# Kernel optimization log

Measured on AMD Instinct MI355X. Metric: run time of the kernel, lower is better.

## Reference

```python
import jax, jax.numpy as jnp
import numpy as np

EMBED = 512
HEADS = 8
HEAD_D = EMBED // HEADS
N = 16
QLEN = 512
KLEN = 512


def _relative_keys(Wr, q_len, k_len):
    # Transformer-XL style sinusoid table of size (q_len + k_len)
    max_dist = q_len + k_len
    inv_freqs = 10000.0 ** (-jnp.arange(0, EMBED, 2, dtype=jnp.float32) / EMBED)
    seq = jnp.arange(max_dist, dtype=jnp.float32)[:, None] * inv_freqs[None, :]
    pos_emb = jnp.concatenate([jnp.sin(seq), jnp.cos(seq)], axis=-1)  # [max_dist, E]
    rel = (pos_emb @ Wr.T).reshape(max_dist, HEADS, HEAD_D)           # [max_dist, H, D]
    # query_offset defaults to key_len
    q_pos = jnp.arange(q_len)[:, None] + k_len
    k_pos = jnp.arange(k_len)[None, :]
    rel_idx = jnp.clip(q_pos - k_pos, 0, max_dist - 1)                # [q, k]
    return rel[rel_idx]                                               # [q, k, H, D]


def setup_inputs() -> dict:
    key = jax.random.key(0)
    ks = jax.random.split(key, 12)
    s = 0.02
    return {
        "values": jax.random.normal(ks[0], (N, KLEN, EMBED), jnp.float32),
        "keys": jax.random.normal(ks[1], (N, KLEN, EMBED), jnp.float32),
        "query": jax.random.normal(ks[2], (N, QLEN, EMBED), jnp.float32),
        "mask": jnp.ones((N, QLEN, KLEN), jnp.int32),
        "Wv": jax.random.normal(ks[3], (HEAD_D, HEAD_D), jnp.float32) * s,
        "Wk": jax.random.normal(ks[4], (HEAD_D, HEAD_D), jnp.float32) * s,
        "Wq": jax.random.normal(ks[5], (HEAD_D, HEAD_D), jnp.float32) * s,
        "Wr": jax.random.normal(ks[6], (EMBED, EMBED), jnp.float32) * s,
        "u_bias": jax.random.normal(ks[7], (HEADS, HEAD_D), jnp.float32) * s,
        "v_bias": jax.random.normal(ks[8], (HEADS, HEAD_D), jnp.float32) * s,
        "Wo": jax.random.normal(ks[9], (EMBED, EMBED), jnp.float32) * s,
        "bo": jnp.zeros((EMBED,), jnp.float32),
    }


def reference(values, keys, query, mask, Wv, Wk, Wq, Wr, u_bias, v_bias, Wo, bo):
    # per-head projections (same D x D weight shared across heads, torch Linear: x @ W.T)
    v = values.reshape(N, KLEN, HEADS, HEAD_D) @ Wv.T
    k = keys.reshape(N, KLEN, HEADS, HEAD_D) @ Wk.T
    q = query.reshape(N, QLEN, HEADS, HEAD_D) @ Wq.T

    rel_keys = _relative_keys(Wr, QLEN, KLEN)  # [q, k, H, D]

    content = jnp.einsum("nqhd,nkhd->nhqk", q + u_bias, k)
    position = jnp.einsum("nqhd,qkhd->nhqk", q + v_bias, rel_keys)
    energy = content + position
    energy = jnp.where(mask[:, None, :, :] == 0, jnp.float32(-1e20), energy)

    attn = jax.nn.softmax(energy / (float(HEAD_D) ** 0.5), axis=3)  # [N,H,q,k]
    out = jnp.einsum("nhqk,nkhd->nqhd", attn, v).reshape(N, QLEN, EMBED)
    out = out @ Wo.T + bo
    return out, attn
```

## Files before the change

kernel.cpp:

```cpp
#include <hip/hip_runtime.h>
#include <math.h>

#define NB     16
#define HEADS  8
#define HD     64
#define EMBED  512
#define QL     512
#define KL     512

#define WS_QU   0
#define WS_QV   2097152
#define WS_KB   4194304
#define WS_VT   6291456
#define WS_PEB  8388608
#define WS_RELB 8912896
#define WS_OH   9175040

typedef __attribute__((ext_vector_type(8))) short bf16x8;
typedef __attribute__((ext_vector_type(4))) float f32x4;
typedef __attribute__((ext_vector_type(8))) unsigned short ushort8v;
typedef __attribute__((ext_vector_type(4))) unsigned short ushort4v;

#define MFMA16 __builtin_amdgcn_mfma_f32_16x16x32_bf16

static __device__ __forceinline__ unsigned short f2bf(float x) {
    unsigned u = __builtin_bit_cast(unsigned, x);
    u += 0x7fffu + ((u >> 16) & 1u);
    return (unsigned short)(u >> 16);
}

__global__ void pe_kernel(unsigned short* __restrict__ peb) {
    int j = blockIdx.x;
    int i = threadIdx.x;
    float invf = exp2f(-(float)i * (13.287712379549449f / 256.0f));
    float ang  = (float)j * invf;
    peb[j * 512 + i]       = f2bf(sinf(ang));
    peb[j * 512 + 256 + i] = f2bf(cosf(ang));
}

__global__ __launch_bounds__(256) void rel_kernel(const unsigned short* __restrict__ peb,
                                                  const float* __restrict__ Wr,
                                                  unsigned short* __restrict__ relb) {
    __shared__ __align__(16) unsigned short At[64][64];
    __shared__ __align__(16) unsigned short Bt[64][64];
    int bm = blockIdx.x >> 3, bn = blockIdx.x & 7;
    int tid = threadIdx.x;
    int w = tid >> 6, lane = tid & 63;
    int fr = lane & 15, fg = lane >> 4;
    f32x4 acc[4] = {};
    for (int kk = 0; kk < 512; kk += 64) {
        __syncthreads();
        for (int p = 0; p < 2; ++p) {
            int idx = tid + 256 * p;
            int row = idx >> 3, slot = idx & 7;
            *(bf16x8*)&At[row][((slot ^ (row & 7))) * 8] =
                *(const bf16x8*)&peb[(bm * 64 + row) * 512 + kk + slot * 8];
        }
        for (int p = 0; p < 4; ++p) {
            int idx = tid + 256 * p;
            int row = idx >> 4, c4 = idx & 15;
            float4 v = *(const float4*)&Wr[(bn * 64 + row) * 512 + kk + c4 * 4];
            ushort4v pk;
            pk[0] = f2bf(v.x); pk[1] = f2bf(v.y); pk[2] = f2bf(v.z); pk[3] = f2bf(v.w);
            int slot = c4 >> 1, rem = (c4 & 1) * 4;
            *(ushort4v*)&Bt[row][((slot ^ (row & 7))) * 8 + rem] = pk;
        }
        __syncthreads();
        bf16x8 af[2];
        int ar = w * 16 + fr;
#pragma unroll
        for (int s = 0; s < 2; ++s)
            af[s] = *(const bf16x8*)&At[ar][((fg + 4 * s) ^ (ar & 7)) * 8];
#pragma unroll
        for (int c = 0; c < 4; ++c) {
            int br = c * 16 + fr;
#pragma unroll
            for (int s = 0; s < 2; ++s) {
                bf16x8 bf = *(const bf16x8*)&Bt[br][((fg + 4 * s) ^ (br & 7)) * 8];
                acc[c] = MFMA16(af[s], bf, acc[c], 0, 0, 0);
            }
        }
    }
#pragma unroll
    for (int c = 0; c < 4; ++c)
#pragma unroll
        for (int i = 0; i < 4; ++i)
            relb[(bn * 1024 + bm * 64 + w * 16 + fg * 4 + i) * 64 + c * 16 + fr] =
                f2bf(acc[c][i]);
}

__global__ __launch_bounds__(256) void proj_kernel(const float* __restrict__ query,
                                                   const float* __restrict__ keys,
                                                   const float* __restrict__ values,
                                                   const float* __restrict__ Wq,
                                                   const float* __restrict__ Wk,
                                                   const float* __restrict__ Wv,
                                                   const float* __restrict__ u_bias,
                                                   const float* __restrict__ v_bias,
                                                   float* __restrict__ ws) {
    __shared__ __align__(16) unsigned short inb[32][512];
    __shared__ __align__(16) unsigned short Wb[3][64][64];
    __shared__ __align__(16) unsigned short vtile[4][64][36];
    int n = blockIdx.x >> 4, t0 = (blockIdx.x & 15) * 32;
    int tid = threadIdx.x;
    int w = tid >> 6, lane = tid & 63;
    int fr = lane & 15, fg = lane >> 4;

    for (int p = 0; p < 3; ++p) {
        const float* Wp = (p == 0) ? Wq : (p == 1) ? Wk : Wv;
        for (int it = 0; it < 4; ++it) {
            int idx = tid + 256 * it;
            int row = idx >> 4, c4 = idx & 15;
            float4 v = *(const float4*)&Wp[row * 64 + c4 * 4];
            ushort4v pk;
            pk[0] = f2bf(v.x); pk[1] = f2bf(v.y); pk[2] = f2bf(v.z); pk[3] = f2bf(v.w);
            int slot = c4 >> 1, rem = (c4 & 1) * 4;
            *(ushort4v*)&Wb[p][row][((slot ^ (row & 7))) * 8 + rem] = pk;
        }
    }
    unsigned short* qu_b = (unsigned short*)(ws + WS_QU);
    unsigned short* qv_b = (unsigned short*)(ws + WS_QV);
    unsigned short* k_b  = (unsigned short*)(ws + WS_KB);
    unsigned short* vT_b = (unsigned short*)(ws + WS_VT);

    for (int p = 0; p < 3; ++p) {
        const float* src = (p == 0) ? query : (p == 1) ? keys : values;
        __syncthreads();
        for (int it = 0; it < 16; ++it) {
            int idx = tid + 256 * it;
            int row = idx >> 7, c4 = idx & 127;
            float4 v = *(const float4*)&src[((long)(n * 512 + t0 + row)) * 512 + c4 * 4];
            ushort4v pk;
            pk[0] = f2bf(v.x); pk[1] = f2bf(v.y); pk[2] = f2bf(v.z); pk[3] = f2bf(v.w);
            int slot = c4 >> 1, rem = (c4 & 1) * 4;
            *(ushort4v*)&inb[row][((slot ^ (row & 7))) * 8 + rem] = pk;
        }
        __syncthreads();
        for (int hh = 0; hh < 2; ++hh) {
            int h = w * 2 + hh, nh = n * 8 + h;
            bf16x8 af[2][2];
#pragma unroll
            for (int tt = 0; tt < 2; ++tt) {
                int ar = tt * 16 + fr;
#pragma unroll
                for (int s = 0; s < 2; ++s)
                    af[tt][s] = *(const bf16x8*)&inb[ar][(h * 8 + ((fg + 4 * s) ^ (ar & 7))) * 8];
            }
            f32x4 acc[2][4] = {};
#pragma unroll
            for (int dt = 0; dt < 4; ++dt) {
                int br = dt * 16 + fr;
                bf16x8 bf[2];
#pragma unroll
                for (int s = 0; s < 2; ++s)
                    bf[s] = *(const bf16x8*)&Wb[p][br][((fg + 4 * s) ^ (br & 7)) * 8];
#pragma unroll
                for (int tt = 0; tt < 2; ++tt)
#pragma unroll
                    for (int s = 0; s < 2; ++s)
                        acc[tt][dt] = MFMA16(af[tt][s], bf[s], acc[tt][dt], 0, 0, 0);
            }
            if (p == 0) {
#pragma unroll
                for (int dt = 0; dt < 4; ++dt) {
                    float ub = u_bias[h * 64 + dt * 16 + fr];
                    float vb = v_bias[h * 64 + dt * 16 + fr];
#pragma unroll
                    for (int tt = 0; tt < 2; ++tt)
#pragma unroll
                        for (int i = 0; i < 4; ++i) {
                            long o = ((long)(nh * 512 + t0 + tt * 16 + fg * 4 + i)) * 64 +
                                     dt * 16 + fr;
                            qu_b[o] = f2bf(acc[tt][dt][i] + ub);
                            qv_b[o] = f2bf(acc[tt][dt][i] + vb);
                        }
                }
            } else if (p == 1) {
#pragma unroll
                for (int dt = 0; dt < 4; ++dt)
#pragma unroll
                    for (int tt = 0; tt < 2; ++tt)
#pragma unroll
                        for (int i = 0; i < 4; ++i)
                            k_b[((long)(nh * 512 + t0 + tt * 16 + fg * 4 + i)) * 64 +
                                dt * 16 + fr] = f2bf(acc[tt][dt][i]);
            } else {
#pragma unroll
                for (int dt = 0; dt < 4; ++dt)
#pragma unroll
                    for (int tt = 0; tt < 2; ++tt)
#pragma unroll
                        for (int i = 0; i < 4; ++i)
                            vtile[w][dt * 16 + fr][tt * 16 + fg * 4 + i] =
                                f2bf(acc[tt][dt][i]);
                __syncthreads();
#pragma unroll
                for (int dg = 0; dg < 8; ++dg) {
                    int d = dg * 8 + (lane >> 3), tq = lane & 7;
                    *(ushort4v*)&vT_b[((long)(nh * 64 + d)) * 512 + t0 + tq * 4] =
                        *(const ushort4v*)&vtile[w][d][tq * 4];
                }
                __syncthreads();
            }
        }
    }
}

__global__ __launch_bounds__(512) void attn_kernel(float* __restrict__ ws,
                                                   const int* __restrict__ mask,
                                                   float* __restrict__ d_out) {
    __shared__ __align__(16) float S[32][516];

    const unsigned short* qu_b = (const unsigned short*)(ws + WS_QU);
    const unsigned short* qv_b = (const unsigned short*)(ws + WS_QV);
    const unsigned short* k_b  = (const unsigned short*)(ws + WS_KB);
    const unsigned short* vT_b = (const unsigned short*)(ws + WS_VT);
    const unsigned short* relb = (const unsigned short*)(ws + WS_RELB);
    unsigned short* ohb = (unsigned short*)(ws + WS_OH);
    float* attn = d_out + 4194304;

    int blk = blockIdx.x;
    int n  = blk >> 7;
    int h  = (blk >> 4) & 7;
    int q0 = (blk & 15) * 32;
    int nh = n * 8 + h;

    int tid  = threadIdx.x;
    int w    = tid >> 6, lane = tid & 63;
    int fr   = lane & 15, fg = lane >> 4;

    bf16x8 quf[2][2], qvf[2][2];
#pragma unroll
    for (int qt = 0; qt < 2; ++qt) {
        long qb = ((long)(nh * 512 + q0 + qt * 16 + fr)) * 64;
#pragma unroll
        for (int s = 0; s < 2; ++s) {
            quf[qt][s] = *(const bf16x8*)&qu_b[qb + (fg + 4 * s) * 8];
            qvf[qt][s] = *(const bf16x8*)&qv_b[qb + (fg + 4 * s) * 8];
        }
    }

    {
        const unsigned short* kbase = k_b + (long)nh * 512 * 64;
        f32x4 acc[2][4] = {};
#pragma unroll
        for (int t = 0; t < 4; ++t) {
            int kcol = w * 64 + t * 16 + fr;
            const unsigned short* kp = kbase + (long)kcol * 64;
            bf16x8 b0 = *(const bf16x8*)&kp[fg * 8];
            bf16x8 b1 = *(const bf16x8*)&kp[(fg + 4) * 8];
#pragma unroll
            for (int qt = 0; qt < 2; ++qt) {
                acc[qt][t] = MFMA16(quf[qt][0], b0, acc[qt][t], 0, 0, 0);
                acc[qt][t] = MFMA16(quf[qt][1], b1, acc[qt][t], 0, 0, 0);
            }
        }
#pragma unroll
        for (int qt = 0; qt < 2; ++qt)
#pragma unroll
            for (int t = 0; t < 4; ++t) {
                int kcol = w * 64 + t * 16 + fr;
                int rb = qt * 16 + fg * 4;
#pragma unroll
                for (int i = 0; i < 4; ++i) S[rb + i][kcol] = acc[qt][t][i];
            }
    }
    __syncthreads();

    {
        const unsigned short* rbase = relb + (long)h * 1024 * 64;
        for (int jt = w; jt < 34; jt += 8) {
            int jj = jt * 16 + fr;
            int j = q0 + 1 + jj;
            const unsigned short* rp = rbase + (long)j * 64;
            bf16x8 b0 = *(const bf16x8*)&rp[fg * 8];
            bf16x8 b1 = *(const bf16x8*)&rp[(fg + 4) * 8];
#pragma unroll
            for (int qt = 0; qt < 2; ++qt) {
                f32x4 acc = {0.f, 0.f, 0.f, 0.f};
                acc = MFMA16(qvf[qt][0], b0, acc, 0, 0, 0);
                acc = MFMA16(qvf[qt][1], b1, acc, 0, 0, 0);
#pragma unroll
                for (int i = 0; i < 4; ++i) {
                    int r = qt * 16 + fg * 4 + i;
                    int k = r + 511 - jj;
                    if ((unsigned)k < 512u) S[r][k] += acc[i];
                }
            }
        }
    }
    __syncthreads();

    for (int rr = 0; rr < 4; ++rr) {
        int r = w * 4 + rr;
        const int* mrow = mask + ((long)(n * 512 + q0 + r)) * 512;
        float lg[8];
        float mx = -3.0e38f;
#pragma unroll
        for (int j = 0; j < 8; ++j) {
            int k = lane + 64 * j;
            float s = S[r][k];
            int m = mrow[k];
            float l = (m == 0) ? -1.25e19f : s * 0.125f;
            lg[j] = l;
            mx = fmaxf(mx, l);
        }
        for (int o = 32; o > 0; o >>= 1) mx = fmaxf(mx, __shfl_xor(mx, o, 64));
        float sum = 0.f;
#pragma unroll
        for (int j = 0; j < 8; ++j) { lg[j] = __expf(lg[j] - mx); sum += lg[j]; }
        for (int o = 32; o > 0; o >>= 1) sum += __shfl_xor(sum, o, 64);
        float inv = 1.0f / sum;
        float* arow = attn + ((long)(nh * 512 + q0 + r)) * 512;
#pragma unroll
        for (int j = 0; j < 8; ++j) {
            int k = lane + 64 * j;
            float p = lg[j] * inv;
            S[r][k] = p;
            arow[k] = p;
        }
    }
    __syncthreads();

    {
        int qt = w & 1, dt = w >> 1;
        const unsigned short* vp0 = vT_b + ((long)(nh * 64 + dt * 16 + fr)) * 512;
        f32x4 oacc = {0.f, 0.f, 0.f, 0.f};
#pragma unroll
        for (int kk = 0; kk < 16; ++kk) {
            const float* sp = &S[qt * 16 + fr][kk * 32 + fg * 8];
            f32x4 a = *(const f32x4*)sp;
            f32x4 b = *(const f32x4*)(sp + 4);
            bf16x8 pk;
            pk[0] = f2bf(a.x); pk[1] = f2bf(a.y); pk[2] = f2bf(a.z); pk[3] = f2bf(a.w);
            pk[4] = f2bf(b.x); pk[5] = f2bf(b.y); pk[6] = f2bf(b.z); pk[7] = f2bf(b.w);
            bf16x8 bf = *(const bf16x8*)&vp0[kk * 32 + fg * 8];
            oacc = MFMA16(pk, bf, oacc, 0, 0, 0);
        }
#pragma unroll
        for (int i = 0; i < 4; ++i)
            ohb[((long)(n * 512 + q0 + qt * 16 + fg * 4 + i)) * 512 +
                h * 64 + dt * 16 + fr] = f2bf(oacc[i]);
    }
}

__global__ __launch_bounds__(256) void wo_kernel(const float* __restrict__ ws,
                                                 const float* __restrict__ Wo,
                                                 const float* __restrict__ bo,
                                                 float* __restrict__ d_out) {
    __shared__ __align__(16) unsigned short At[128][64];
    __shared__ __align__(16) unsigned short Bt[64][64];
    const unsigned short* ohb = (const unsigned short*)(ws + WS_OH);
    int bm = blockIdx.x >> 3, bn = blockIdx.x & 7;
    int tid = threadIdx.x;
    int w = tid >> 6, lane = tid & 63;
    int fr = lane & 15, fg = lane >> 4;
    f32x4 acc[2][4] = {};
    for (int kk = 0; kk < 512; kk += 64) {
        __syncthreads();
        for (int p = 0; p < 4; ++p) {
            int idx = tid + 256 * p;
            int row = idx >> 3, slot = idx & 7;
            *(bf16x8*)&At[row][((slot ^ (row & 7))) * 8] =
                *(const bf16x8*)&ohb[(long)(bm * 128 + row) * 512 + kk + slot * 8];
        }
        for (int p = 0; p < 2; ++p) {
            int idx = tid + 256 * p;
            int row = idx >> 3, slot = idx & 7;
            const float* g = &Wo[(bn * 64 + row) * 512 + kk + slot * 8];
            float4 a = *(const float4*)g;
            float4 b = *(const float4*)(g + 4);
            ushort8v pk;
            pk[0] = f2bf(a.x); pk[1] = f2bf(a.y); pk[2] = f2bf(a.z); pk[3] = f2bf(a.w);
            pk[4] = f2bf(b.x); pk[5] = f2bf(b.y); pk[6] = f2bf(b.z); pk[7] = f2bf(b.w);
            *(ushort8v*)&Bt[row][((slot ^ (row & 7))) * 8] = pk;
        }
        __syncthreads();
        bf16x8 af[2][2], bfr[4][2];
#pragma unroll
        for (int t = 0; t < 2; ++t) {
            int ar = w * 32 + t * 16 + fr;
#pragma unroll
            for (int s = 0; s < 2; ++s)
                af[t][s] = *(const bf16x8*)&At[ar][((fg + s * 4) ^ (ar & 7)) * 8];
        }
#pragma unroll
        for (int c = 0; c < 4; ++c) {
            int br = c * 16 + fr;
#pragma unroll
            for (int s = 0; s < 2; ++s)
                bfr[c][s] = *(const bf16x8*)&Bt[br][((fg + s * 4) ^ (br & 7)) * 8];
        }
#pragma unroll
        for (int t = 0; t < 2; ++t)
#pragma unroll
            for (int c = 0; c < 4; ++c)
#pragma unroll
                for (int s = 0; s < 2; ++s)
                    acc[t][c] = MFMA16(af[t][s], bfr[c][s], acc[t][c], 0, 0, 0);
    }
#pragma unroll
    for (int t = 0; t < 2; ++t)
#pragma unroll
        for (int c = 0; c < 4; ++c) {
            int col = bn * 64 + c * 16 + fr;
            float b = bo[col];
#pragma unroll
            for (int i = 0; i < 4; ++i) {
                int row = bm * 128 + w * 32 + t * 16 + fg * 4 + i;
                d_out[(long)row * 512 + col] = acc[t][c][i] + b;
            }
        }
}

extern "C" void kernel_launch(void* const* d_in, const int* in_sizes, int n_in,
                              void* d_out, int out_size, void* d_ws, size_t ws_size,
                              hipStream_t stream) {
    const float* values = (const float*)d_in[0];
    const float* keys   = (const float*)d_in[1];
    const float* query  = (const float*)d_in[2];
    const int*   mask   = (const int*)d_in[3];
    const float* Wv     = (const float*)d_in[4];
    const float* Wk     = (const float*)d_in[5];
    const float* Wq     = (const float*)d_in[6];
    const float* Wr     = (const float*)d_in[7];
    const float* u_bias = (const float*)d_in[8];
    const float* v_bias = (const float*)d_in[9];
    const float* Wo     = (const float*)d_in[10];
    const float* bo     = (const float*)d_in[11];
    float* out = (float*)d_out;
    float* ws  = (float*)d_ws;

    unsigned short* peb  = (unsigned short*)(ws + WS_PEB);
    unsigned short* relb = (unsigned short*)(ws + WS_RELB);

    hipLaunchKernelGGL(pe_kernel,   dim3(1024),  dim3(256), 0, stream, peb);
    hipLaunchKernelGGL(rel_kernel,  dim3(128),   dim3(256), 0, stream, peb, Wr, relb);
    hipLaunchKernelGGL(proj_kernel, dim3(256),   dim3(256), 0, stream,
                       query, keys, values, Wq, Wk, Wv, u_bias, v_bias, ws);
    hipLaunchKernelGGL(attn_kernel, dim3(2048),  dim3(512), 0, stream, ws, mask, out);
    hipLaunchKernelGGL(wo_kernel,   dim3(512),   dim3(256), 0, stream, ws, Wo, bo, out);
}
```

Baseline: 147.2 us.

## Halve attention query tile to 16 rows, split PV over key halves, vectorize softmax

Result: slower. 173.3 us (+17.7%).

```diff
diff --git a/kernel.cpp b/kernel.cpp
--- a/kernel.cpp
+++ b/kernel.cpp
@@ -27,6 +27,15 @@
     unsigned u = __builtin_bit_cast(unsigned, x);
     u += 0x7fffu + ((u >> 16) & 1u);
     return (unsigned short)(u >> 16);
+}
+
+static __device__ __forceinline__ bf16x8 pack8(f32x4 a, f32x4 b) {
+    union { bf16x8 v; unsigned u[4]; } r;
+    asm("v_cvt_pk_bf16_f32 %0, %1, %2" : "=v"(r.u[0]) : "v"(a[0]), "v"(a[1]));
+    asm("v_cvt_pk_bf16_f32 %0, %1, %2" : "=v"(r.u[1]) : "v"(a[2]), "v"(a[3]));
+    asm("v_cvt_pk_bf16_f32 %0, %1, %2" : "=v"(r.u[2]) : "v"(b[0]), "v"(b[1]));
+    asm("v_cvt_pk_bf16_f32 %0, %1, %2" : "=v"(r.u[3]) : "v"(b[2]), "v"(b[3]));
+    return r.v;
 }
 
 __global__ void pe_kernel(unsigned short* __restrict__ peb) {
@@ -209,7 +218,8 @@
 __global__ __launch_bounds__(512) void attn_kernel(float* __restrict__ ws,
                                                    const int* __restrict__ mask,
                                                    float* __restrict__ d_out) {
-    __shared__ __align__(16) float S[32][516];
+    __shared__ __align__(16) float S[16][516];
+    __shared__ __align__(16) float red[4][16][17];
 
     const unsigned short* qu_b = (const unsigned short*)(ws + WS_QU);
     const unsigned short* qv_b = (const unsigned short*)(ws + WS_QV);
@@ -219,128 +229,129 @@
     unsigned short* ohb = (unsigned short*)(ws + WS_OH);
     float* attn = d_out + 4194304;
 
-    int blk = blockIdx.x;
-    int n  = blk >> 7;
-    int h  = (blk >> 4) & 7;
-    int q0 = (blk & 15) * 32;
-    int nh = n * 8 + h;
+    int bid = blockIdx.x;
+    int swz = (bid & 7) * 512 + (bid >> 3);
+    int nh = swz >> 5;
+    int n  = nh >> 3, h = nh & 7;
+    int q0 = (swz & 31) * 16;
 
     int tid  = threadIdx.x;
     int w    = tid >> 6, lane = tid & 63;
     int fr   = lane & 15, fg = lane >> 4;
 
-    bf16x8 quf[2][2], qvf[2][2];
-#pragma unroll
-    for (int qt = 0; qt < 2; ++qt) {
-        long qb = ((long)(nh * 512 + q0 + qt * 16 + fr)) * 64;
+    bf16x8 quf[2], qvf[2];
+    {
+        long qb = ((long)(nh * 512 + q0 + fr)) * 64;
 #pragma unroll
         for (int s = 0; s < 2; ++s) {
-            quf[qt][s] = *(const bf16x8*)&qu_b[qb + (fg + 4 * s) * 8];
-            qvf[qt][s] = *(const bf16x8*)&qv_b[qb + (fg + 4 * s) * 8];
+            quf[s] = *(const bf16x8*)&qu_b[qb + (fg + 4 * s) * 8];
+            qvf[s] = *(const bf16x8*)&qv_b[qb + (fg + 4 * s) * 8];
         }
     }
 
     {
         const unsigned short* kbase = k_b + (long)nh * 512 * 64;
-        f32x4 acc[2][4] = {};
+        f32x4 cacc[4] = {};
 #pragma unroll
         for (int t = 0; t < 4; ++t) {
             int kcol = w * 64 + t * 16 + fr;
             const unsigned short* kp = kbase + (long)kcol * 64;
             bf16x8 b0 = *(const bf16x8*)&kp[fg * 8];
             bf16x8 b1 = *(const bf16x8*)&kp[(fg + 4) * 8];
-#pragma unroll
-            for (int qt = 0; qt < 2; ++qt) {
-                acc[qt][t] = MFMA16(quf[qt][0], b0, acc[qt][t], 0, 0, 0);
-                acc[qt][t] = MFMA16(quf[qt][1], b1, acc[qt][t], 0, 0, 0);
-            }
-        }
-#pragma unroll
-        for (int qt = 0; qt < 2; ++qt)
-#pragma unroll
-            for (int t = 0; t < 4; ++t) {
-                int kcol = w * 64 + t * 16 + fr;
-                int rb = qt * 16 + fg * 4;
-#pragma unroll
-                for (int i = 0; i < 4; ++i) S[rb + i][kcol] = acc[qt][t][i];
-            }
+            cacc[t] = MFMA16(quf[0], b0, cacc[t], 0, 0, 0);
+            cacc[t] = MFMA16(quf[1], b1, cacc[t], 0, 0, 0);
+        }
+#pragma unroll
+        for (int t = 0; t < 4; ++t)
+#pragma unroll
+            for (int i = 0; i < 4; ++i)
+                S[fg * 4 + i][w * 64 + t * 16 + fr] = cacc[t][i];
     }
     __syncthreads();
 
     {
         const unsigned short* rbase = relb + (long)h * 1024 * 64;
-        for (int jt = w; jt < 34; jt += 8) {
+        for (int jt = w; jt < 33; jt += 8) {
             int jj = jt * 16 + fr;
-            int j = q0 + 1 + jj;
+            int j = q0 + 1 + jj; if (j > 1023) j = 1023;
             const unsigned short* rp = rbase + (long)j * 64;
             bf16x8 b0 = *(const bf16x8*)&rp[fg * 8];
             bf16x8 b1 = *(const bf16x8*)&rp[(fg + 4) * 8];
-#pragma unroll
-            for (int qt = 0; qt < 2; ++qt) {
-                f32x4 acc = {0.f, 0.f, 0.f, 0.f};
-                acc = MFMA16(qvf[qt][0], b0, acc, 0, 0, 0);
-                acc = MFMA16(qvf[qt][1], b1, acc, 0, 0, 0);
-#pragma unroll
-                for (int i = 0; i < 4; ++i) {
-                    int r = qt * 16 + fg * 4 + i;
-                    int k = r + 511 - jj;
-                    if ((unsigned)k < 512u) S[r][k] += acc[i];
-                }
+            f32x4 acc = {0.f, 0.f, 0.f, 0.f};
+            acc = MFMA16(qvf[0], b0, acc, 0, 0, 0);
+            acc = MFMA16(qvf[1], b1, acc, 0, 0, 0);
+#pragma unroll
+            for (int i = 0; i < 4; ++i) {
+                int r = fg * 4 + i;
+                int k = r + 511 - jj;
+                if ((unsigned)k < 512u) S[r][k] += acc[i];
             }
         }
     }
     __syncthreads();
 
-    for (int rr = 0; rr < 4; ++rr) {
-        int r = w * 4 + rr;
+    for (int rr = 0; rr < 2; ++rr) {
+        int r = w * 2 + rr;
         const int* mrow = mask + ((long)(n * 512 + q0 + r)) * 512;
+        f32x4 s0 = *(const f32x4*)&S[r][lane * 8];
+        f32x4 s1 = *(const f32x4*)&S[r][lane * 8 + 4];
+        int4 m0 = *(const int4*)&mrow[lane * 8];
+        int4 m1 = *(const int4*)&mrow[lane * 8 + 4];
         float lg[8];
-        float mx = -3.0e38f;
-#pragma unroll
-        for (int j = 0; j < 8; ++j) {
-            int k = lane + 64 * j;
-            float s = S[r][k];
-            int m = mrow[k];
-            float l = (m == 0) ? -1.25e19f : s * 0.125f;
-            lg[j] = l;
-            mx = fmaxf(mx, l);
-        }
+        lg[0] = (m0.x == 0) ? -1.25e19f : s0[0] * 0.125f;
+        lg[1] = (m0.y == 0) ? -1.25e19f : s0[1] * 0.125f;
+        lg[2] = (m0.z == 0) ? -1.25e19f : s0[2] * 0.125f;
+        lg[3] = (m0.w == 0) ? -1.25e19f : s0[3] * 0.125f;
+        lg[4] = (m1.x == 0) ? -1.25e19f : s1[0] * 0.125f;
+        lg[5] = (m1.y == 0) ? -1.25e19f : s1[1] * 0.125f;
+        lg[6] = (m1.z == 0) ? -1.25e19f : s1[2] * 0.125f;
+        lg[7] = (m1.w == 0) ? -1.25e19f : s1[3] * 0.125f;
+        float mx = lg[0];
+#pragma unroll
+        for (int j = 1; j < 8; ++j) mx = fmaxf(mx, lg[j]);
         for (int o = 32; o > 0; o >>= 1) mx = fmaxf(mx, __shfl_xor(mx, o, 64));
         float sum = 0.f;
 #pragma unroll
         for (int j = 0; j < 8; ++j) { lg[j] = __expf(lg[j] - mx); sum += lg[j]; }
         for (int o = 32; o > 0; o >>= 1) sum += __shfl_xor(sum, o, 64);
         float inv = 1.0f / sum;
+        f32x4 p0 = {lg[0] * inv, lg[1] * inv, lg[2] * inv, lg[3] * inv};
+        f32x4 p1 = {lg[4] * inv, lg[5] * inv, lg[6] * inv, lg[7] * inv};
+        *(f32x4*)&S[r][lane * 8]     = p0;
+        *(f32x4*)&S[r][lane * 8 + 4] = p1;
         float* arow = attn + ((long)(nh * 512 + q0 + r)) * 512;
-#pragma unroll
-        for (int j = 0; j < 8; ++j) {
-            int k = lane + 64 * j;
-            float p = lg[j] * inv;
-            S[r][k] = p;
-            arow[k] = p;
-        }
+        *(f32x4*)&arow[lane * 8]     = p0;
+        *(f32x4*)&arow[lane * 8 + 4] = p1;
     }
     __syncthreads();
 
     {
-        int qt = w & 1, dt = w >> 1;
-        const unsigned short* vp0 = vT_b + ((long)(nh * 64 + dt * 16 + fr)) * 512;
+        int dt = w & 3, kh = w >> 2;
+        const unsigned short* vp0 =
+            vT_b + ((long)(nh * 64 + dt * 16 + fr)) * 512 + kh * 256;
         f32x4 oacc = {0.f, 0.f, 0.f, 0.f};
 #pragma unroll
-        for (int kk = 0; kk < 16; ++kk) {
-            const float* sp = &S[qt * 16 + fr][kk * 32 + fg * 8];
+        for (int kk = 0; kk < 8; ++kk) {
+            const float* sp = &S[fr][kh * 256 + kk * 32 + fg * 8];
             f32x4 a = *(const f32x4*)sp;
             f32x4 b = *(const f32x4*)(sp + 4);
-            bf16x8 pk;
-            pk[0] = f2bf(a.x); pk[1] = f2bf(a.y); pk[2] = f2bf(a.z); pk[3] = f2bf(a.w);
-            pk[4] = f2bf(b.x); pk[5] = f2bf(b.y); pk[6] = f2bf(b.z); pk[7] = f2bf(b.w);
+            bf16x8 pk = pack8(a, b);
             bf16x8 bf = *(const bf16x8*)&vp0[kk * 32 + fg * 8];
             oacc = MFMA16(pk, bf, oacc, 0, 0, 0);
         }
-#pragma unroll
-        for (int i = 0; i < 4; ++i)
-            ohb[((long)(n * 512 + q0 + qt * 16 + fg * 4 + i)) * 512 +
-                h * 64 + dt * 16 + fr] = f2bf(oacc[i]);
+        if (kh == 1) {
+#pragma unroll
+            for (int i = 0; i < 4; ++i) red[dt][fg * 4 + i][fr] = oacc[i];
+        }
+        __syncthreads();
+        if (kh == 0) {
+#pragma unroll
+            for (int i = 0; i < 4; ++i) {
+                float o = oacc[i] + red[dt][fg * 4 + i][fr];
+                ohb[((long)(n * 512 + q0 + fg * 4 + i)) * 512 +
+                    h * 64 + dt * 16 + fr] = f2bf(o);
+            }
+        }
     }
 }
 
@@ -438,6 +449,6 @@
     hipLaunchKernelGGL(rel_kernel,  dim3(128),   dim3(256), 0, stream, peb, Wr, relb);
     hipLaunchKernelGGL(proj_kernel, dim3(256),   dim3(256), 0, stream,
                        query, keys, values, Wq, Wk, Wv, u_bias, v_bias, ws);
-    hipLaunchKernelGGL(attn_kernel, dim3(2048),  dim3(512), 0, stream, ws, mask, out);
+    hipLaunchKernelGGL(attn_kernel, dim3(4096),  dim3(512), 0, stream, ws, mask, out);
     hipLaunchKernelGGL(wo_kernel,   dim3(512),   dim3(256), 0, stream, ws, Wo, bo, out);
 }
```

## Persist K/V in registers across four query tiles per attention block

Applied to the files above, without the earlier changes.

New measurement: 146.4 us. Within noise of the previous version (-0.6%).

```diff
diff --git a/kernel.cpp b/kernel.cpp
--- a/kernel.cpp
+++ b/kernel.cpp
@@ -27,6 +27,15 @@
     unsigned u = __builtin_bit_cast(unsigned, x);
     u += 0x7fffu + ((u >> 16) & 1u);
     return (unsigned short)(u >> 16);
+}
+
+static __device__ __forceinline__ bf16x8 pack8(f32x4 a, f32x4 b) {
+    union { bf16x8 v; unsigned u[4]; } r;
+    asm("v_cvt_pk_bf16_f32 %0, %1, %2" : "=v"(r.u[0]) : "v"(a[0]), "v"(a[1]));
+    asm("v_cvt_pk_bf16_f32 %0, %1, %2" : "=v"(r.u[1]) : "v"(a[2]), "v"(a[3]));
+    asm("v_cvt_pk_bf16_f32 %0, %1, %2" : "=v"(r.u[2]) : "v"(b[0]), "v"(b[1]));
+    asm("v_cvt_pk_bf16_f32 %0, %1, %2" : "=v"(r.u[3]) : "v"(b[2]), "v"(b[3]));
+    return r.v;
 }
 
 __global__ void pe_kernel(unsigned short* __restrict__ peb) {
@@ -210,6 +219,7 @@
                                                    const int* __restrict__ mask,
                                                    float* __restrict__ d_out) {
     __shared__ __align__(16) float S[32][516];
+    __shared__ __align__(16) float red[4][32][17];
 
     const unsigned short* qu_b = (const unsigned short*)(ws + WS_QU);
     const unsigned short* qv_b = (const unsigned short*)(ws + WS_QV);
@@ -219,128 +229,147 @@
     unsigned short* ohb = (unsigned short*)(ws + WS_OH);
     float* attn = d_out + 4194304;
 
-    int blk = blockIdx.x;
-    int n  = blk >> 7;
-    int h  = (blk >> 4) & 7;
-    int q0 = (blk & 15) * 32;
-    int nh = n * 8 + h;
+    int bid = blockIdx.x;
+    int swz = (bid & 7) * 64 + (bid >> 3);
+    int nh = swz >> 2, qb = swz & 3;
+    int n  = nh >> 3, h = nh & 7;
 
     int tid  = threadIdx.x;
     int w    = tid >> 6, lane = tid & 63;
     int fr   = lane & 15, fg = lane >> 4;
 
-    bf16x8 quf[2][2], qvf[2][2];
-#pragma unroll
-    for (int qt = 0; qt < 2; ++qt) {
-        long qb = ((long)(nh * 512 + q0 + qt * 16 + fr)) * 64;
-#pragma unroll
-        for (int s = 0; s < 2; ++s) {
-            quf[qt][s] = *(const bf16x8*)&qu_b[qb + (fg + 4 * s) * 8];
-            qvf[qt][s] = *(const bf16x8*)&qv_b[qb + (fg + 4 * s) * 8];
-        }
-    }
-
-    {
-        const unsigned short* kbase = k_b + (long)nh * 512 * 64;
-        f32x4 acc[2][4] = {};
-#pragma unroll
-        for (int t = 0; t < 4; ++t) {
-            int kcol = w * 64 + t * 16 + fr;
-            const unsigned short* kp = kbase + (long)kcol * 64;
-            bf16x8 b0 = *(const bf16x8*)&kp[fg * 8];
-            bf16x8 b1 = *(const bf16x8*)&kp[(fg + 4) * 8];
+    const unsigned short* kbase = k_b + (long)nh * 512 * 64;
+    bf16x8 kreg[4][2];
+#pragma unroll
+    for (int t = 0; t < 4; ++t) {
+        const unsigned short* kp = kbase + (long)(w * 64 + t * 16 + fr) * 64;
+        kreg[t][0] = *(const bf16x8*)&kp[fg * 8];
+        kreg[t][1] = *(const bf16x8*)&kp[(fg + 4) * 8];
+    }
+    int dt = w & 3, kh = w >> 2;
+    const unsigned short* vp0 = vT_b + ((long)(nh * 64 + dt * 16 + fr)) * 512 + kh * 256;
+    bf16x8 vreg[8];
+#pragma unroll
+    for (int kk = 0; kk < 8; ++kk)
+        vreg[kk] = *(const bf16x8*)&vp0[kk * 32 + fg * 8];
+
+    const unsigned short* rbase = relb + (long)h * 1024 * 64;
+
+    for (int ti = 0; ti < 4; ++ti) {
+        int q0 = qb * 128 + ti * 32;
+
+#pragma unroll
+        for (int qt = 0; qt < 2; ++qt) {
+            long qa = ((long)(nh * 512 + q0 + qt * 16 + fr)) * 64;
+            bf16x8 a0 = *(const bf16x8*)&qu_b[qa + fg * 8];
+            bf16x8 a1 = *(const bf16x8*)&qu_b[qa + (fg + 4) * 8];
+#pragma unroll
+            for (int t = 0; t < 4; ++t) {
+                f32x4 acc = {0.f, 0.f, 0.f, 0.f};
+                acc = MFMA16(a0, kreg[t][0], acc, 0, 0, 0);
+                acc = MFMA16(a1, kreg[t][1], acc, 0, 0, 0);
+                int kcol = w * 64 + t * 16 + fr;
+#pragma unroll
+                for (int i = 0; i < 4; ++i)
+                    S[qt * 16 + fg * 4 + i][kcol] = acc[i];
+            }
+        }
+        __syncthreads();
+
+        {
+            bf16x8 qvf[2][2];
 #pragma unroll
             for (int qt = 0; qt < 2; ++qt) {
-                acc[qt][t] = MFMA16(quf[qt][0], b0, acc[qt][t], 0, 0, 0);
-                acc[qt][t] = MFMA16(quf[qt][1], b1, acc[qt][t], 0, 0, 0);
-            }
-        }
-#pragma unroll
-        for (int qt = 0; qt < 2; ++qt)
-#pragma unroll
-            for (int t = 0; t < 4; ++t) {
-                int kcol = w * 64 + t * 16 + fr;
-                int rb = qt * 16 + fg * 4;
-#pragma unroll
-                for (int i = 0; i < 4; ++i) S[rb + i][kcol] = acc[qt][t][i];
-            }
-    }
-    __syncthreads();
-
-    {
-        const unsigned short* rbase = relb + (long)h * 1024 * 64;
-        for (int jt = w; jt < 34; jt += 8) {
-            int jj = jt * 16 + fr;
-            int j = q0 + 1 + jj;
-            const unsigned short* rp = rbase + (long)j * 64;
-            bf16x8 b0 = *(const bf16x8*)&rp[fg * 8];
-            bf16x8 b1 = *(const bf16x8*)&rp[(fg + 4) * 8];
-#pragma unroll
-            for (int qt = 0; qt < 2; ++qt) {
-                f32x4 acc = {0.f, 0.f, 0.f, 0.f};
-                acc = MFMA16(qvf[qt][0], b0, acc, 0, 0, 0);
-                acc = MFMA16(qvf[qt][1], b1, acc, 0, 0, 0);
-#pragma unroll
-                for (int i = 0; i < 4; ++i) {
-                    int r = qt * 16 + fg * 4 + i;
-                    int k = r + 511 - jj;
-                    if ((unsigned)k < 512u) S[r][k] += acc[i];
+                long qa = ((long)(nh * 512 + q0 + qt * 16 + fr)) * 64;
+                qvf[qt][0] = *(const bf16x8*)&qv_b[qa + fg * 8];
+                qvf[qt][1] = *(const bf16x8*)&qv_b[qa + (fg + 4) * 8];
+            }
+            for (int jt = w; jt < 34; jt += 8) {
+                int jj = jt * 16 + fr;
+                int j = q0 + 1 + jj;
+                const unsigned short* rp = rbase + (long)j * 64;
+                bf16x8 b0 = *(const bf16x8*)&rp[fg * 8];
+                bf16x8 b1 = *(const bf16x8*)&rp[(fg + 4) * 8];
+#pragma unroll
+                for (int qt = 0; qt < 2; ++qt) {
+                    f32x4 acc = {0.f, 0.f, 0.f, 0.f};
+                    acc = MFMA16(qvf[qt][0], b0, acc, 0, 0, 0);
+                    acc = MFMA16(qvf[qt][1], b1, acc, 0, 0, 0);
+#pragma unroll
+                    for (int i = 0; i < 4; ++i) {
+                        int r = qt * 16 + fg * 4 + i;
+                        int k = r + 511 - jj;
+                        if ((unsigned)k < 512u) S[r][k] += acc[i];
+                    }
                 }
             }
         }
-    }
-    __syncthreads();
-
-    for (int rr = 0; rr < 4; ++rr) {
-        int r = w * 4 + rr;
-        const int* mrow = mask + ((long)(n * 512 + q0 + r)) * 512;
-        float lg[8];
-        float mx = -3.0e38f;
-#pragma unroll
-        for (int j = 0; j < 8; ++j) {
-            int k = lane + 64 * j;
-            float s = S[r][k];
-            int m = mrow[k];
-            float l = (m == 0) ? -1.25e19f : s * 0.125f;
-            lg[j] = l;
-            mx = fmaxf(mx, l);
-        }
-        for (int o = 32; o > 0; o >>= 1) mx = fmaxf(mx, __shfl_xor(mx, o, 64));
-        float sum = 0.f;
-#pragma unroll
-        for (int j = 0; j < 8; ++j) { lg[j] = __expf(lg[j] - mx); sum += lg[j]; }
-        for (int o = 32; o > 0; o >>= 1) sum += __shfl_xor(sum, o, 64);
-        float inv = 1.0f / sum;
-        float* arow = attn + ((long)(nh * 512 + q0 + r)) * 512;
-#pragma unroll
-        for (int j = 0; j < 8; ++j) {
-            int k = lane + 64 * j;
-            float p = lg[j] * inv;
-            S[r][k] = p;
-            arow[k] = p;
-        }
-    }
-    __syncthreads();
-
-    {
-        int qt = w & 1, dt = w >> 1;
-        const unsigned short* vp0 = vT_b + ((long)(nh * 64 + dt * 16 + fr)) * 512;
-        f32x4 oacc = {0.f, 0.f, 0.f, 0.f};
-#pragma unroll
-        for (int kk = 0; kk < 16; ++kk) {
-            const float* sp = &S[qt * 16 + fr][kk * 32 + fg * 8];
-            f32x4 a = *(const f32x4*)sp;
-            f32x4 b = *(const f32x4*)(sp + 4);
-            bf16x8 pk;
-            pk[0] = f2bf(a.x); pk[1] = f2bf(a.y); pk[2] = f2bf(a.z); pk[3] = f2bf(a.w);
-            pk[4] = f2bf(b.x); pk[5] = f2bf(b.y); pk[6] = f2bf(b.z); pk[7] = f2bf(b.w);
-            bf16x8 bf = *(const bf16x8*)&vp0[kk * 32 + fg * 8];
-            oacc = MFMA16(pk, bf, oacc, 0, 0, 0);
-        }
-#pragma unroll
-        for (int i = 0; i < 4; ++i)
-            ohb[((long)(n * 512 + q0 + qt * 16 + fg * 4 + i)) * 512 +
-                h * 64 + dt * 16 + fr] = f2bf(oacc[i]);
+        __syncthreads();
+
+        for (int rr = 0; rr < 4; ++rr) {
+            int r = w * 4 + rr;
+            const int* mrow = mask + ((long)(n * 512 + q0 + r)) * 512;
+            float lg[8];
+            float mx = -3.0e38f;
+#pragma unroll
+            for (int j = 0; j < 8; ++j) {
+                int k = lane + 64 * j;
+                float s = S[r][k];
+                int m = mrow[k];
+                float l = (m == 0) ? -1.25e19f : s * 0.125f;
+                lg[j] = l;
+                mx = fmaxf(mx, l);
+            }
+            for (int o = 32; o > 0; o >>= 1) mx = fmaxf(mx, __shfl_xor(mx, o, 64));
+            float sum = 0.f;
+#pragma unroll
+            for (int j = 0; j < 8; ++j) { lg[j] = __expf(lg[j] - mx); sum += lg[j]; }
+            for (int o = 32; o > 0; o >>= 1) sum += __shfl_xor(sum, o, 64);
+            float inv = 1.0f / sum;
+            float* arow = attn + ((long)(nh * 512 + q0 + r)) * 512;
+#pragma unroll
+            for (int j = 0; j < 8; ++j) {
+                int k = lane + 64 * j;
+                float p = lg[j] * inv;
+                S[r][k] = p;
+                arow[k] = p;
+            }
+        }
+        __syncthreads();
+
+        {
+            f32x4 oacc[2] = {{0.f,0.f,0.f,0.f},{0.f,0.f,0.f,0.f}};
+#pragma unroll
+            for (int kk = 0; kk < 8; ++kk) {
+#pragma unroll
+                for (int qt = 0; qt < 2; ++qt) {
+                    const float* sp = &S[qt * 16 + fr][kh * 256 + kk * 32 + fg * 8];
+                    f32x4 a = *(const f32x4*)sp;
+                    f32x4 b = *(const f32x4*)(sp + 4);
+                    bf16x8 pk = pack8(a, b);
+                    oacc[qt] = MFMA16(pk, vreg[kk], oacc[qt], 0, 0, 0);
+                }
+            }
+            if (kh == 1) {
+#pragma unroll
+                for (int qt = 0; qt < 2; ++qt)
+#pragma unroll
+                    for (int i = 0; i < 4; ++i)
+                        red[dt][qt * 16 + fg * 4 + i][fr] = oacc[qt][i];
+            }
+            __syncthreads();
+            if (kh == 0) {
+#pragma unroll
+                for (int qt = 0; qt < 2; ++qt)
+#pragma unroll
+                    for (int i = 0; i < 4; ++i) {
+                        float o = oacc[qt][i] + red[dt][qt * 16 + fg * 4 + i][fr];
+                        ohb[((long)(n * 512 + q0 + qt * 16 + fg * 4 + i)) * 512 +
+                            h * 64 + dt * 16 + fr] = f2bf(o);
+                    }
+            }
+        }
+        __syncthreads();
     }
 }
 
@@ -438,6 +467,6 @@
     hipLaunchKernelGGL(rel_kernel,  dim3(128),   dim3(256), 0, stream, peb, Wr, relb);
     hipLaunchKernelGGL(proj_kernel, dim3(256),   dim3(256), 0, stream,
                        query, keys, values, Wq, Wk, Wv, u_bias, v_bias, ws);
-    hipLaunchKernelGGL(attn_kernel, dim3(2048),  dim3(512), 0, stream, ws, mask, out);
+    hipLaunchKernelGGL(attn_kernel, dim3(512),   dim3(512), 0, stream, ws, mask, out);
     hipLaunchKernelGGL(wo_kernel,   dim3(512),   dim3(256), 0, stream, ws, Wo, bo, out);
 }
```
